# Kernel tuning notes

Measured on AMD Instinct MI355X. Metric: run time of the kernel, lower is better.

## Reference

```python
import jax, jax.numpy as jnp
from jax import lax
import numpy as np

HEAD_SIZE = 64
D_MIX = 32
D_DECAY = 64
D_GATE = 64


def setup_inputs() -> dict:
    key = jax.random.key(0)
    B, T, C = 4, 2048, 1024
    H = C // HEAD_SIZE
    ks = jax.random.split(key, 24)
    n = lambda i, shape, s=1.0: (jax.random.normal(ks[i], shape, dtype=jnp.float32) * s)
    return {
        "x": n(0, (B, T, C)),
        "maa_x": n(1, (C,), 0.1), "maa_w": n(2, (C,), 0.1), "maa_k": n(3, (C,), 0.1),
        "maa_v": n(4, (C,), 0.1), "maa_r": n(5, (C,), 0.1), "maa_g": n(6, (C,), 0.1),
        "maa_w1": n(7, (C, 5 * D_MIX), 0.01), "maa_w2": n(8, (5, D_MIX, C), 0.01),
        "Wr": n(9, (C, C), C ** -0.5), "Wk": n(10, (C, C), C ** -0.5),
        "Wv": n(11, (C, C), C ** -0.5), "Wo": n(12, (C, C), C ** -0.5),
        "gate_w1": n(13, (C, D_GATE), 0.01), "gate_w2": n(14, (D_GATE, C), 0.01),
        "time_decay": n(15, (C,), 1.0) - 4.0,
        "decay_w1": n(16, (C, D_DECAY), 0.01), "decay_w2": n(17, (D_DECAY, C), 0.01),
        "u": n(18, (H, HEAD_SIZE), 0.1),
        "ln_g": jnp.ones((C,), jnp.float32), "ln_b": jnp.zeros((C,), jnp.float32),
    }


def _wkv6(r, k, v, w, u):
    # r,k,v: [B,T,C]; w: decay (already exp(-exp(.))) [B,T,C]; u: [H,N]
    B, T, C = r.shape
    N = HEAD_SIZE
    H = C // N
    to_h = lambda a: a.reshape(B, T, H, N).transpose(1, 0, 2, 3)  # [T,B,H,N]
    rT, kT, vT, wT = map(to_h, (r, k, v, w))

    def step(S, inp):  # S: [B,H,N,N] (key_dim i x value_dim j)
        rt, kt, vt, wt = inp
        kv = kt[..., :, None] * vt[..., None, :]            # [B,H,N,N]
        y = jnp.einsum('bhi,bhij->bhj', rt, S + u[None, :, :, None] * kv)
        S = wt[..., None] * S + kv
        return S, y

    S0 = jnp.zeros((B, H, N, N), r.dtype)
    _, y = lax.scan(step, S0, (rT, kT, vT, wT))
    return y.transpose(1, 0, 2, 3).reshape(B, T, C)


def reference(x, maa_x, maa_w, maa_k, maa_v, maa_r, maa_g, maa_w1, maa_w2,
              Wr, Wk, Wv, Wo, gate_w1, gate_w2, time_decay, decay_w1, decay_w2,
              u, ln_g, ln_b):
    B, T, C = x.shape
    H, N = C // HEAD_SIZE, HEAD_SIZE
    # time shift: prepend zero row, drop last (ZeroPad2d((0,0,1,-1)))
    xx = jnp.concatenate([jnp.zeros_like(x[:, :1]), x[:, :-1]], axis=1) - x
    xxx = x + xx * maa_x
    lora = jnp.tanh(xxx @ maa_w1).reshape(B, T, 5, D_MIX)
    m = jnp.einsum('btfd,fdc->fbtc', lora, maa_w2)  # [5,B,T,C]
    mw, mk, mv, mr, mg = m[0], m[1], m[2], m[3], m[4]
    xw = x + xx * (maa_w + mw)
    xk = x + xx * (maa_k + mk)
    xv = x + xx * (maa_v + mv)
    xr = x + xx * (maa_r + mr)
    xg = x + xx * (maa_g + mg)
    r = xr @ Wr
    k = xk @ Wk
    v = xv @ Wv
    g = jnp.tanh(xg @ gate_w1) @ gate_w2
    w = time_decay + jnp.tanh(xw @ decay_w1) @ decay_w2
    wdec = jnp.exp(-jnp.exp(w))  # decay applied inside the CUDA kernel
    y = _wkv6(r, k, v, wdec, u)
    # GroupNorm over heads, eps = 1e-5 * HEAD_SIZE_DIVISOR**2 = 6.4e-4
    yh = y.reshape(B, T, H, N)
    mu = yh.mean(-1, keepdims=True)
    var = yh.var(-1, keepdims=True)
    yn = ((yh - mu) / jnp.sqrt(var + 6.4e-4)).reshape(B, T, C) * ln_g + ln_b
    return (yn * g) @ Wo
```

## Files before the change

### kernel.cpp

```cpp
#include <hip/hip_runtime.h>
#include <hip/hip_bf16.h>
#include <stdint.h>

typedef __hip_bfloat16 bf16;
typedef __attribute__((ext_vector_type(8))) short bf16x8;
typedef __attribute__((ext_vector_type(4))) float f32x4;

#define CC 1024
#define TT 2048
#define BB 4
#define BT 8192
#define HH 16
#define NN 64

#define MFMA(a, b, c) __builtin_amdgcn_mfma_f32_16x16x32_bf16(a, b, c, 0, 0, 0)

#define GLD(g, l) __builtin_amdgcn_global_load_lds( \
    (const __attribute__((address_space(1))) void*)(g), \
    (__attribute__((address_space(3))) void*)(l), 16, 0, 0)

__device__ __forceinline__ short f2bs(float f) {
    bf16 h = __float2bfloat16(f);
    return *reinterpret_cast<short*>(&h);
}
__device__ __forceinline__ float bs2f(short s) {
    bf16 h = *reinterpret_cast<bf16*>(&s);
    return __bfloat162float(h);
}

template <typename EPI>
__device__ __forceinline__ void gemm128(short* As, short* Bs,
                                        const bf16* __restrict__ A, int lda,
                                        const bf16* __restrict__ Bt, int ldb,
                                        int kiters, int m0, int n0, EPI epi)
{
    const int tid = threadIdx.x;
    const int l   = tid & 63, wv = tid >> 6;
    const int wm  = wv >> 1, wn = wv & 1;
    const int q   = l >> 4, lr = l & 15;
    const int row = tid & 127, kg1 = tid >> 7;

    f32x4 acc[4][4] = {};

    const bf16* ga = A  + (size_t)(m0 + row) * lda + kg1 * 8;
    const bf16* gb = Bt + (size_t)(n0 + row) * ldb + kg1 * 8;
    short* la1 = As + tid * 8;
    short* la2 = As + (tid + 256) * 8;
    short* lb1 = Bs + tid * 8;
    short* lb2 = Bs + (tid + 256) * 8;

    for (int kb = 0; kb < kiters; ++kb) {
        __syncthreads();
        const bf16* gak = ga + kb * 32;
        const bf16* gbk = gb + kb * 32;
        GLD(gak,      la1);
        GLD(gak + 16, la2);
        GLD(gbk,      lb1);
        GLD(gbk + 16, lb2);
        __syncthreads();
        bf16x8 af[4], bfb[4];
#pragma unroll
        for (int mt = 0; mt < 4; ++mt)
            af[mt] = *(const bf16x8*)(As + (q * 128 + wm * 64 + mt * 16 + lr) * 8);
#pragma unroll
        for (int nt = 0; nt < 4; ++nt)
            bfb[nt] = *(const bf16x8*)(Bs + (q * 128 + wn * 64 + nt * 16 + lr) * 8);
#pragma unroll
        for (int mt = 0; mt < 4; ++mt)
#pragma unroll
            for (int nt = 0; nt < 4; ++nt)
                acc[mt][nt] = MFMA(af[mt], bfb[nt], acc[mt][nt]);
    }
#pragma unroll
    for (int mt = 0; mt < 4; ++mt)
#pragma unroll
        for (int nt = 0; nt < 4; ++nt)
#pragma unroll
            for (int rr = 0; rr < 4; ++rr)
                epi(m0 + wm * 64 + mt * 16 + q * 4 + rr,
                    n0 + wn * 64 + nt * 16 + lr, acc[mt][nt][rr]);
}

template <typename EPI>
__device__ __forceinline__ void gemm128k64(short* As, short* Bs,
                                           const bf16* __restrict__ A, int lda,
                                           const bf16* __restrict__ Bt, int ldb,
                                           int kiters, int m0, int n0, EPI epi)
{
    const int tid = threadIdx.x;
    const int l   = tid & 63, wv = tid >> 6;
    const int wm  = wv >> 1, wn = wv & 1;
    const int q   = l >> 4, lr = l & 15;
    const int row = tid & 127, kg1 = tid >> 7;

    f32x4 acc[4][4] = {};

    const bf16* ga = A  + (size_t)(m0 + row) * lda + kg1 * 8;
    const bf16* gb = Bt + (size_t)(n0 + row) * ldb + kg1 * 8;

    for (int kb = 0; kb < kiters; ++kb) {
        __syncthreads();
        const bf16* gak = ga + kb * 64;
        const bf16* gbk = gb + kb * 64;
        GLD(gak,      As + tid * 8);
        GLD(gak + 16, As + (tid + 256) * 8);
        GLD(gak + 32, As + (tid + 512) * 8);
        GLD(gak + 48, As + (tid + 768) * 8);
        GLD(gbk,      Bs + tid * 8);
        GLD(gbk + 16, Bs + (tid + 256) * 8);
        GLD(gbk + 32, Bs + (tid + 512) * 8);
        GLD(gbk + 48, Bs + (tid + 768) * 8);
        __syncthreads();
        bf16x8 af[2][4], bfb[2][4];
#pragma unroll
        for (int hh = 0; hh < 2; ++hh) {
#pragma unroll
            for (int mt = 0; mt < 4; ++mt)
                af[hh][mt] = *(const bf16x8*)(As +
                    ((q + hh * 4) * 128 + wm * 64 + mt * 16 + lr) * 8);
#pragma unroll
            for (int nt = 0; nt < 4; ++nt)
                bfb[hh][nt] = *(const bf16x8*)(Bs +
                    ((q + hh * 4) * 128 + wn * 64 + nt * 16 + lr) * 8);
        }
#pragma unroll
        for (int mt = 0; mt < 4; ++mt)
#pragma unroll
            for (int nt = 0; nt < 4; ++nt) {
                acc[mt][nt] = MFMA(af[0][mt], bfb[0][nt], acc[mt][nt]);
                acc[mt][nt] = MFMA(af[1][mt], bfb[1][nt], acc[mt][nt]);
            }
    }
#pragma unroll
    for (int mt = 0; mt < 4; ++mt)
#pragma unroll
        for (int nt = 0; nt < 4; ++nt)
#pragma unroll
            for (int rr = 0; rr < 4; ++rr)
                epi(m0 + wm * 64 + mt * 16 + q * 4 + rr,
                    n0 + wn * 64 + nt * 16 + lr, acc[mt][nt][rr]);
}

__global__ __launch_bounds__(256) void k_prep_all(
    const float* __restrict__ Wr, const float* __restrict__ Wk,
    const float* __restrict__ Wv, const float* __restrict__ Wo,
    const float* __restrict__ maa_w1, const float* __restrict__ gate_w1,
    const float* __restrict__ decay_w1, const float* __restrict__ gate_w2,
    const float* __restrict__ decay_w2, const float* __restrict__ maa_w2,
    const float* __restrict__ mw, const float* __restrict__ mk,
    const float* __restrict__ mv, const float* __restrict__ mr,
    const float* __restrict__ mg, const float* __restrict__ x,
    const float* __restrict__ maa_x,
    bf16* __restrict__ WT3, bf16* __restrict__ WoT, bf16* __restrict__ w1T,
    bf16* __restrict__ w1T2, bf16* __restrict__ w2T2, bf16* __restrict__ w2T5,
    float* __restrict__ maas, bf16* __restrict__ xxx,
    bf16* __restrict__ xb, bf16* __restrict__ xxb)
{
    __shared__ float tile[32][33];
    int idx = blockIdx.x;
    if (idx >= 4900) {
        size_t i = ((size_t)(idx - 4900) * 256 + threadIdx.x) * 4;
        int cc = i & (CC - 1);
        int t  = (i >> 10) & (TT - 1);
        float4 xm = *(const float4*)(x + i);
        float4 xp = t ? *(const float4*)(x + i - CC)
                      : make_float4(0.f, 0.f, 0.f, 0.f);
        float4 ax = *(const float4*)(maa_x + cc);
        float xxv[4] = {xp.x - xm.x, xp.y - xm.y, xp.z - xm.z, xp.w - xm.w};
        float xmv[4] = {xm.x, xm.y, xm.z, xm.w};
        float axv[4] = {ax.x, ax.y, ax.z, ax.w};
#pragma unroll
        for (int e = 0; e < 4; ++e) {
            xb[i + e]  = __float2bfloat16(xmv[e]);
            xxb[i + e] = __float2bfloat16(xxv[e]);
            xxx[i + e] = __float2bfloat16(xmv[e] + xxv[e] * axv[e]);
        }
        return;
    }
    const float* src; bf16* dst; int rows, cols_in, tx_;
    if (idx < 4096) {
        int s = idx >> 10; idx &= 1023;
        src = (s == 0) ? Wr : (s == 1) ? Wk : (s == 2) ? Wv : Wo;
        dst = (s == 3) ? WoT : WT3 + (size_t)s * CC * CC;
        rows = CC; cols_in = CC; tx_ = 32;
    } else if (idx < 4352) { idx -= 4096; src = maa_w1;  dst = w1T;  rows = CC; cols_in = 160; tx_ = 8; }
    else if (idx < 4480)   { idx -= 4352; src = gate_w1; dst = w1T2; rows = CC; cols_in = 64;  tx_ = 4; }
    else if (idx < 4608)   { idx -= 4480; src = decay_w1; dst = w1T2 + 128 * CC; rows = CC; cols_in = 64; tx_ = 4; }
    else if (idx < 4672)   { idx -= 4608; src = gate_w2;  dst = w2T2;           rows = 64; cols_in = CC; tx_ = 32; }
    else if (idx < 4736)   { idx -= 4672; src = decay_w2; dst = w2T2 + CC * 64; rows = 64; cols_in = CC; tx_ = 32; }
    else if (idx < 4896)   { idx -= 4736; int f = idx >> 5; idx &= 31;
                             src = maa_w2 + (size_t)f * 32 * CC;
                             dst = w2T5 + (size_t)f * CC * 32; rows = 32; cols_in = CC; tx_ = 32; }
    else {
        int i = (idx - 4896) * 256 + threadIdx.x;
        if (i < CC) {
            maas[i]          = mw[i];
            maas[CC + i]     = mk[i];
            maas[2 * CC + i] = mv[i];
            maas[3 * CC + i] = mr[i];
            maas[4 * CC + i] = mg[i];
        }
        return;
    }
    int bx = idx % tx_, by = idx / tx_;
    int c0 = bx * 32, r0 = by * 32;
    int tx = threadIdx.x & 31, ty = threadIdx.x >> 5;
    for (int i = ty; i < 32; i += 8) {
        int cc2 = c0 + tx;
        tile[i][tx] = (cc2 < cols_in) ? src[(size_t)(r0 + i) * cols_in + cc2] : 0.f;
    }
    __syncthreads();
    for (int i = ty; i < 32; i += 8)
        dst[(size_t)(c0 + i) * rows + r0 + tx] = __float2bfloat16(tile[tx][i]);
}

__global__ __launch_bounds__(256) void g_lora(const bf16* __restrict__ xxx,
                                              const bf16* __restrict__ w1T,
                                              bf16* __restrict__ L)
{
    __shared__ __align__(16) short lds[8192];
    int m0 = blockIdx.x * 128, n0 = blockIdx.y * 128;
    gemm128(lds, lds + 4096, xxx, CC, w1T, CC, CC / 32, m0, n0,
            [&](int m, int n, float v) {
                if (n < 160) L[(size_t)m * 160 + n] = __float2bfloat16(tanhf(v));
            });
}

__global__ __launch_bounds__(256) void g_xvar(const bf16* __restrict__ L,
                                              const bf16* __restrict__ w2T,
                                              const float* __restrict__ maas,
                                              const bf16* __restrict__ xb,
                                              const bf16* __restrict__ xxb,
                                              bf16* __restrict__ xvars)
{
    __shared__ __align__(16) short lds[8192];
    int m0 = blockIdx.x * 128, n0 = blockIdx.y * 128;
    for (int f = 0; f < 5; ++f) {
        const bf16* A  = L + f * 32;
        const bf16* Bt = w2T + (size_t)f * CC * 32;
        const float* maa = maas + f * CC;
        bf16* out = xvars + (size_t)f * BT * CC;
        gemm128(lds, lds + 4096, A, 160, Bt, 32, 1, m0, n0,
                [&](int m, int n, float v) {
                    float xm = __bfloat162float(xb[(size_t)m * CC + n]);
                    float xx = __bfloat162float(xxb[(size_t)m * CC + n]);
                    out[(size_t)m * CC + n] =
                        __float2bfloat16(xm + xx * (maa[n] + v));
                });
    }
}

__global__ __launch_bounds__(256) void g_rkv5(const bf16* __restrict__ xvars,
                                              const bf16* __restrict__ WT,
                                              const bf16* __restrict__ w1T2,
                                              bf16* __restrict__ rkv,
                                              bf16* __restrict__ hid)
{
    __shared__ __align__(16) short lds[16384];
    int z = blockIdx.z;
    int m0 = blockIdx.x * 128;
    if (blockIdx.y < 8) {
        int n0 = blockIdx.y * 128;
        int f = (z == 0) ? 3 : z;
        const bf16* A  = xvars + (size_t)f * BT * CC;
        const bf16* Bt = WT + (size_t)z * CC * CC;
        bf16* out = rkv + (size_t)z * BT * CC;
        gemm128k64(lds, lds + 8192, A, CC, Bt, CC, CC / 64, m0, n0,
                   [&](int m, int n, float v) {
                       out[(size_t)m * CC + n] = __float2bfloat16(v);
                   });
    } else {
        if (z == 2) return;
        int zz = z;
        const bf16* A  = xvars + (size_t)(zz == 0 ? 4 : 0) * BT * CC;
        const bf16* Bt = w1T2 + (size_t)zz * 128 * CC;
        bf16* out = hid + (size_t)zz * BT * 64;
        gemm128k64(lds, lds + 8192, A, CC, Bt, CC, CC / 64, m0, 0,
                   [&](int m, int n, float v) {
                       if (n < 64) out[(size_t)m * 64 + n] = __float2bfloat16(tanhf(v));
                   });
    }
}

__global__ __launch_bounds__(256) void k_wkv_p1(const bf16* __restrict__ r,
                                                const bf16* __restrict__ kk,
                                                const bf16* __restrict__ vv,
                                                const bf16* __restrict__ hidW,
                                                const bf16* __restrict__ w2d,
                                                const float* __restrict__ td,
                                                const float* __restrict__ u,
                                                bf16* __restrict__ y,
                                                bf16* __restrict__ RTg,
                                                short* __restrict__ Mg,
                                                float* __restrict__ plg)
{
    constexpr int PW = 65, PB = 72;
    __shared__ __align__(16) char smem[16640 + 3 * 9216 + 768];
    float* LW = (float*)smem;
    short* VT = (short*)smem;
    short* RT = (short*)(smem + 16640);
    short* KT = (short*)(smem + 16640 + 9216);
    short* AT = KT;
    short* KH = (short*)(smem + 16640 + 2 * 9216);
    short* HT = KT;
    short* WD = KH;
    float* SU = (float*)(smem + 16640 + 3 * 9216);
    float* SD = SU + 64;

    const int tid = threadIdx.x;
    const int lane = tid & 63, wq = tid >> 6;
    const int row = tid >> 2, g = tid & 3, j0 = g * 16;
    const int l15 = lane & 15, q = lane >> 4;
    const int bh = blockIdx.x >> 5, c = blockIdx.x & 31;
    const int b = bh >> 4, h = bh & 15;
    const size_t base = (size_t)b * TT * CC + (size_t)h * NN;
    const int t0 = c * 64;
    const int bt0 = b * TT + t0;
    const size_t cb = (size_t)blockIdx.x * 4096;

    if (tid < 64) SU[tid] = u[h * NN + tid];

#pragma unroll
    for (int rnd = 0; rnd < 2; ++rnd) {
        int ee = rnd * 256 + tid;
        int rw = ee >> 3, c8 = (ee & 7) * 8;
        *(bf16x8*)(HT + rw * PB + c8) =
            *(const bf16x8*)(hidW + (size_t)(bt0 + rw) * 64 + c8);
        *(bf16x8*)(WD + rw * PB + c8) =
            *(const bf16x8*)(w2d + (size_t)(h * 64 + rw) * 64 + c8);
    }
    const size_t gb = base + (size_t)(t0 + row) * CC + j0;
    bf16x8 r0 = *(const bf16x8*)(r + gb),  r1 = *(const bf16x8*)(r + gb + 8);
    bf16x8 k0 = *(const bf16x8*)(kk + gb), k1 = *(const bf16x8*)(kk + gb + 8);
    bf16x8 v0 = *(const bf16x8*)(vv + gb), v1 = *(const bf16x8*)(vv + gb + 8);
    float tdv[4];
#pragma unroll
    for (int ct = 0; ct < 4; ++ct) tdv[ct] = td[h * 64 + ct * 16 + l15];
    __syncthreads();
    {
        bf16x8 aH0 = *(const bf16x8*)(HT + (wq * 16 + l15) * PB + q * 8);
        bf16x8 aH1 = *(const bf16x8*)(HT + (wq * 16 + l15) * PB + q * 8 + 32);
        f32x4 lwa[4] = {};
#pragma unroll
        for (int ct = 0; ct < 4; ++ct) {
            bf16x8 bW0 = *(const bf16x8*)(WD + (ct * 16 + l15) * PB + q * 8);
            bf16x8 bW1 = *(const bf16x8*)(WD + (ct * 16 + l15) * PB + q * 8 + 32);
            lwa[ct] = MFMA(aH0, bW0, lwa[ct]);
            lwa[ct] = MFMA(aH1, bW1, lwa[ct]);
        }
#pragma unroll
        for (int ct = 0; ct < 4; ++ct)
#pragma unroll
            for (int rr = 0; rr < 4; ++rr) {
                int t = wq * 16 + q * 4 + rr, j = ct * 16 + l15;
                LW[t * PW + j] = -expf(tdv[ct] + lwa[ct][rr]);
            }
    }
    __syncthreads();
    for (int jj = 0; jj < 16; ++jj) {
        int j = wq * 16 + jj;
        float xv = LW[lane * PW + j];
#pragma unroll
        for (int d = 1; d < 64; d <<= 1) {
            float t2 = __shfl_up(xv, d);
            if (lane >= d) xv += t2;
        }
        LW[lane * PW + j] = xv;
    }
    __syncthreads();
    float rF[16], kF[16];
#pragma unroll
    for (int c2 = 0; c2 < 8; ++c2) {
        rF[c2] = bs2f(r0[c2]); rF[8 + c2] = bs2f(r1[c2]);
        kF[c2] = bs2f(k0[c2]); kF[8 + c2] = bs2f(k1[c2]);
    }
    float cwp[16], cwm[16], cwL[16];
#pragma unroll
    for (int c2 = 0; c2 < 16; ++c2) {
        cwp[c2] = LW[row * PW + j0 + c2];
        cwm[c2] = row ? LW[(row - 1) * PW + j0 + c2] : 0.f;
        cwL[c2] = LW[63 * PW + j0 + c2];
    }
    bf16x8 w0, w1;
#pragma unroll
    for (int c2 = 0; c2 < 8; ++c2) {
        w0[c2] = f2bs(rF[c2] * expf(cwm[c2]));
        w1[c2] = f2bs(rF[8 + c2] * expf(cwm[8 + c2]));
    }
    *(bf16x8*)(RT + row * PB + j0)     = w0;
    *(bf16x8*)(RT + row * PB + j0 + 8) = w1;
    *(bf16x8*)((short*)RTg + cb + row * 64 + j0)     = w0;
    *(bf16x8*)((short*)RTg + cb + row * 64 + j0 + 8) = w1;
#pragma unroll
    for (int c2 = 0; c2 < 8; ++c2) {
        w0[c2] = f2bs(kF[c2] * expf(-cwp[c2]));
        w1[c2] = f2bs(kF[8 + c2] * expf(-cwp[8 + c2]));
    }
    *(bf16x8*)(KT + row * PB + j0)     = w0;
    *(bf16x8*)(KT + row * PB + j0 + 8) = w1;
#pragma unroll
    for (int c2 = 0; c2 < 16; ++c2)
        KH[(j0 + c2) * PB + row] = f2bs(kF[c2] * expf(cwL[c2] - cwp[c2]));
    if (tid < 64) plg[(size_t)blockIdx.x * 64 + tid] = expf(LW[63 * PW + tid]);
    float dpart = 0.f;
#pragma unroll
    for (int c2 = 0; c2 < 16; ++c2)
        dpart = fmaf(rF[c2] * kF[c2], SU[j0 + c2], dpart);
    dpart += __shfl_xor(dpart, 1);
    dpart += __shfl_xor(dpart, 2);
    if (g == 0) SD[row] = dpart;
    __syncthreads();
#pragma unroll
    for (int c2 = 0; c2 < 8; ++c2) {
        VT[(j0 + c2) * PB + row]     = v0[c2];
        VT[(j0 + 8 + c2) * PB + row] = v1[c2];
    }
    bf16x8 aF0 = *(const bf16x8*)(RT + (wq * 16 + l15) * PB + q * 8);
    bf16x8 aF1 = *(const bf16x8*)(RT + (wq * 16 + l15) * PB + q * 8 + 32);
    f32x4 Am[4] = {};
#pragma unroll
    for (int ct = 0; ct < 4; ++ct) {
        bf16x8 bF0 = *(const bf16x8*)(KT + (ct * 16 + l15) * PB + q * 8);
        bf16x8 bF1 = *(const bf16x8*)(KT + (ct * 16 + l15) * PB + q * 8 + 32);
        Am[ct] = MFMA(aF0, bF0, Am[ct]);
        Am[ct] = MFMA(aF1, bF1, Am[ct]);
    }
    __syncthreads();
#pragma unroll
    for (int ct = 0; ct < 4; ++ct)
#pragma unroll
        for (int rr = 0; rr < 4; ++rr) {
            int s = wq * 16 + q * 4 + rr, p = ct * 16 + l15;
            float vA = Am[ct][rr];
            vA = (p > s) ? 0.f : (p == s ? SD[s] : vA);
            AT[s * PB + p] = f2bs(vA);
        }
    __syncthreads();
    f32x4 Y[4] = {}, M[4] = {};
    bf16x8 aA0 = *(const bf16x8*)(AT + (wq * 16 + l15) * PB + q * 8);
    bf16x8 aA1 = *(const bf16x8*)(AT + (wq * 16 + l15) * PB + q * 8 + 32);
    bf16x8 aV0 = *(const bf16x8*)(VT + (wq * 16 + l15) * PB + q * 8);
    bf16x8 aV1 = *(const bf16x8*)(VT + (wq * 16 + l15) * PB + q * 8 + 32);
#pragma unroll
    for (int ct = 0; ct < 4; ++ct) {
        bf16x8 bV0 = *(const bf16x8*)(VT + (ct * 16 + l15) * PB + q * 8);
        bf16x8 bV1 = *(const bf16x8*)(VT + (ct * 16 + l15) * PB + q * 8 + 32);
        Y[ct] = MFMA(aA0, bV0, Y[ct]);
        Y[ct] = MFMA(aA1, bV1, Y[ct]);
        bf16x8 bK0 = *(const bf16x8*)(KH + (ct * 16 + l15) * PB + q * 8);
        bf16x8 bK1 = *(const bf16x8*)(KH + (ct * 16 + l15) * PB + q * 8 + 32);
        M[ct] = MFMA(aV0, bK0, M[ct]);
        M[ct] = MFMA(aV1, bK1, M[ct]);
    }
#pragma unroll
    for (int ct = 0; ct < 4; ++ct)
#pragma unroll
        for (int rr = 0; rr < 4; ++rr) {
            int s = wq * 16 + q * 4 + rr;
            y[base + (size_t)(t0 + s) * CC + ct * 16 + l15] =
                __float2bfloat16(Y[ct][rr]);
            Mg[cb + (size_t)s * 64 + ct * 16 + l15] = f2bs(M[ct][rr]);
        }
}

__global__ __launch_bounds__(256) void k_wkv_p2(const short* __restrict__ Mg,
                                                const float* __restrict__ plg,
                                                bf16* __restrict__ Sg)
{
    int bh = blockIdx.x >> 4, part = blockIdx.x & 15;
    int i = part * 4 + (threadIdx.x >> 6), j = threadIdx.x & 63;
    float S = 0.f;
    size_t eb = (size_t)bh * 32 * 4096 + (size_t)i * 64 + j;
    size_t pb = (size_t)bh * 32 * 64 + j;
    for (int c = 0; c < 32; ++c) {
        Sg[eb + (size_t)c * 4096] = __float2bfloat16(S);
        S = plg[pb + (size_t)c * 64] * S + bs2f(Mg[eb + (size_t)c * 4096]);
    }
}

__global__ __launch_bounds__(256) void k_wkv_p3(const bf16* __restrict__ RTg,
                                                const bf16* __restrict__ Sg,
                                                const bf16* __restrict__ y,
                                                const bf16* __restrict__ hidG,
                                                const bf16* __restrict__ w2g,
                                                const float* __restrict__ ln_g,
                                                const float* __restrict__ ln_b,
                                                bf16* __restrict__ A2)
{
    constexpr int PB = 72;
    __shared__ __align__(16) short BufA[64 * PB], BufB[64 * PB];
    const int tid = threadIdx.x;
    const int lane = tid & 63, wq = tid >> 6;
    const int l15 = lane & 15, q = lane >> 4;
    const int bh = blockIdx.x >> 5, c = blockIdx.x & 31;
    const int b = bh >> 4, h = bh & 15;
    const int t0 = c * 64;
    const int bt0 = b * TT + t0;
    const size_t cb = (size_t)blockIdx.x * 4096;

#pragma unroll
    for (int rnd = 0; rnd < 2; ++rnd) {
        int ee = rnd * 256 + tid;
        int rw = ee >> 3, c8 = (ee & 7) * 8;
        *(bf16x8*)(BufA + rw * PB + c8) =
            *(const bf16x8*)(hidG + (size_t)(bt0 + rw) * 64 + c8);
        *(bf16x8*)(BufB + rw * PB + c8) =
            *(const bf16x8*)(w2g + (size_t)(h * 64 + rw) * 64 + c8);
    }
    __syncthreads();
    f32x4 G[4] = {};
    {
        bf16x8 aH0 = *(const bf16x8*)(BufA + (wq * 16 + l15) * PB + q * 8);
        bf16x8 aH1 = *(const bf16x8*)(BufA + (wq * 16 + l15) * PB + q * 8 + 32);
#pragma unroll
        for (int ct = 0; ct < 4; ++ct) {
            bf16x8 bW0 = *(const bf16x8*)(BufB + (ct * 16 + l15) * PB + q * 8);
            bf16x8 bW1 = *(const bf16x8*)(BufB + (ct * 16 + l15) * PB + q * 8 + 32);
            G[ct] = MFMA(aH0, bW0, G[ct]);
            G[ct] = MFMA(aH1, bW1, G[ct]);
        }
    }
    __syncthreads();
#pragma unroll
    for (int rnd = 0; rnd < 2; ++rnd) {
        int ee = rnd * 256 + tid;
        int rw = ee >> 3, c8 = (ee & 7) * 8;
        *(bf16x8*)(BufA + rw * PB + c8) =
            *(const bf16x8*)((const short*)RTg + cb + rw * 64 + c8);
        *(bf16x8*)(BufB + rw * PB + c8) =
            *(const bf16x8*)((const short*)Sg + cb + rw * 64 + c8);
    }
    __syncthreads();

    f32x4 Yc[4];
#pragma unroll
    for (int ct = 0; ct < 4; ++ct)
#pragma unroll
        for (int rr = 0; rr < 4; ++rr) {
            int s = wq * 16 + q * 4 + rr;
            Yc[ct][rr] = __bfloat162float(
                y[((size_t)bt0 + s) * CC + h * NN + ct * 16 + l15]);
        }
    bf16x8 aF0 = *(const bf16x8*)(BufA + (wq * 16 + l15) * PB + q * 8);
    bf16x8 aF1 = *(const bf16x8*)(BufA + (wq * 16 + l15) * PB + q * 8 + 32);
#pragma unroll
    for (int ct = 0; ct < 4; ++ct) {
        bf16x8 bS0 = *(const bf16x8*)(BufB + (ct * 16 + l15) * PB + q * 8);
        bf16x8 bS1 = *(const bf16x8*)(BufB + (ct * 16 + l15) * PB + q * 8 + 32);
        Yc[ct] = MFMA(aF0, bS0, Yc[ct]);
        Yc[ct] = MFMA(aF1, bS1, Yc[ct]);
    }
#pragma unroll
    for (int rr = 0; rr < 4; ++rr) {
        float s1 = 0.f, s2 = 0.f;
#pragma unroll
        for (int ct = 0; ct < 4; ++ct) {
            float vA = Yc[ct][rr];
            s1 += vA; s2 += vA * vA;
        }
#pragma unroll
        for (int o = 1; o < 16; o <<= 1) {
            s1 += __shfl_xor(s1, o);
            s2 += __shfl_xor(s2, o);
        }
        float mu  = s1 * (1.f / 64.f);
        float var = s2 * (1.f / 64.f) - mu * mu;
        float rstd = rsqrtf(var + 6.4e-4f);
        int s = wq * 16 + q * 4 + rr;
        size_t mrow = ((size_t)bt0 + s) * CC;
#pragma unroll
        for (int ct = 0; ct < 4; ++ct) {
            int ch = h * NN + ct * 16 + l15;
            float yn = (Yc[ct][rr] - mu) * rstd;
            float out = (yn * ln_g[ch] + ln_b[ch]) * G[ct][rr];
            A2[mrow + ch] = __float2bfloat16(out);
        }
    }
}

__global__ __launch_bounds__(256) void g_out(const bf16* __restrict__ A2,
                                             const bf16* __restrict__ WoT,
                                             float* __restrict__ out)
{
    __shared__ __align__(16) short lds[16384];
    int m0 = blockIdx.x * 128, n0 = blockIdx.y * 128;
    gemm128k64(lds, lds + 8192, A2, CC, WoT, CC, CC / 64, m0, n0,
               [&](int m, int n, float v) { out[(size_t)m * CC + n] = v; });
}

extern "C" void kernel_launch(void* const* d_in, const int* in_sizes, int n_in,
                              void* d_out, int out_size, void* d_ws, size_t ws_size,
                              hipStream_t stream)
{
    const float* x        = (const float*)d_in[0];
    const float* maa_x    = (const float*)d_in[1];
    const float* maa_w    = (const float*)d_in[2];
    const float* maa_k    = (const float*)d_in[3];
    const float* maa_v    = (const float*)d_in[4];
    const float* maa_r    = (const float*)d_in[5];
    const float* maa_g    = (const float*)d_in[6];
    const float* maa_w1   = (const float*)d_in[7];
    const float* maa_w2   = (const float*)d_in[8];
    const float* Wr       = (const float*)d_in[9];
    const float* Wk       = (const float*)d_in[10];
    const float* Wv       = (const float*)d_in[11];
    const float* Wo       = (const float*)d_in[12];
    const float* gate_w1  = (const float*)d_in[13];
    const float* gate_w2  = (const float*)d_in[14];
    const float* time_dec = (const float*)d_in[15];
    const float* decay_w1 = (const float*)d_in[16];
    const float* decay_w2 = (const float*)d_in[17];
    const float* u        = (const float*)d_in[18];
    const float* ln_g     = (const float*)d_in[19];
    const float* ln_b     = (const float*)d_in[20];

    size_t off = 0;
    auto alloc = [&](size_t bytes) {
        off = (off + 255) & ~(size_t)255;
        void* p = (char*)d_ws + off;
        off += bytes;
        return p;
    };
    bf16*  WT3   = (bf16*) alloc(3ull * CC * CC * 2);
    bf16*  WoT   = (bf16*) alloc((size_t)CC * CC * 2);
    bf16*  w1T   = (bf16*) alloc(256ull * CC * 2);
    bf16*  w1T2  = (bf16*) alloc(2ull * 128 * CC * 2);
    bf16*  w2T2  = (bf16*) alloc(2ull * CC * 64 * 2);
    bf16*  w2T5  = (bf16*) alloc(5ull * CC * 32 * 2);
    float* maas  = (float*)alloc(5ull * CC * 4);
    char* bufA = (char*)alloc((size_t)BT * CC * 2);
    bf16* xxxbf = (bf16*)bufA;
    bf16* A2    = (bf16*)bufA;
    char* bufB = (char*)alloc((size_t)BT * 160 * 2);
    bf16* Lbf  = (bf16*)bufB;
    bf16* hid  = (bf16*)bufB;
    char* bufC = (char*)alloc(5ull * BT * CC * 2);
    bf16*  xvars = (bf16*)bufC;
    bf16*  ybuf  = (bf16*)bufC;
    bf16*  RTg   = (bf16*)(bufC + (size_t)BT * CC * 2);
    bf16*  rkv  = (bf16*)alloc(3ull * BT * CC * 2);
    bf16*  Sg   = rkv;
    bf16*  xb   = (bf16*) alloc((size_t)BT * CC * 2);
    bf16*  xxb  = (bf16*) alloc((size_t)BT * CC * 2);
    short* Mg   = (short*)alloc(64ull * 32 * 4096 * 2);
    float* plg  = (float*)alloc(64ull * 32 * 64 * 4);

    k_prep_all<<<dim3(13092), 256, 0, stream>>>(
        Wr, Wk, Wv, Wo, maa_w1, gate_w1, decay_w1, gate_w2, decay_w2, maa_w2,
        maa_w, maa_k, maa_v, maa_r, maa_g, x, maa_x,
        WT3, WoT, w1T, w1T2, w2T2, w2T5, maas, xxxbf, xb, xxb);

    g_lora<<<dim3(64, 2), 256, 0, stream>>>(xxxbf, w1T, Lbf);
    g_xvar<<<dim3(64, 8), 256, 0, stream>>>(Lbf, w2T5, maas, xb, xxb, xvars);
    g_rkv5<<<dim3(64, 9, 3), 256, 0, stream>>>(xvars, WT3, w1T2, rkv, hid);
    k_wkv_p1<<<dim3(2048), 256, 0, stream>>>(rkv, rkv + (size_t)BT * CC,
                                             rkv + 2ull * BT * CC,
                                             hid + (size_t)BT * 64,
                                             w2T2 + CC * 64,
                                             time_dec, u, ybuf, RTg, Mg, plg);
    k_wkv_p2<<<dim3(1024), 256, 0, stream>>>(Mg, plg, Sg);
    k_wkv_p3<<<dim3(2048), 256, 0, stream>>>(RTg, Sg, ybuf,
                                             hid,
                                             w2T2,
                                             ln_g, ln_b, A2);
    g_out<<<dim3(64, 8), 256, 0, stream>>>(A2, WoT, (float*)d_out);
}
```

Baseline: 419.3 us.

## Double-buffer LDS tiles in k64 GEMM to overlap loads with MFMA

Turns the 128x128x64 GEMM main loop into a two-stage software pipeline. The next k-tile is issued via global_load_lds into an alternate LDS buffer while MFMAs run on the current one, and the MFMA block runs at raised wave priority via s_setprio. This is meant to hide global-load latency and cut one barrier per iteration. In exchange LDS per block doubles to 64KB, which may reduce occupancy for the rkv and output GEMMs.

```diff
diff --git a/kernel.cpp b/kernel.cpp
--- a/kernel.cpp
+++ b/kernel.cpp
@@ -98,31 +98,42 @@
     const bf16* ga = A  + (size_t)(m0 + row) * lda + kg1 * 8;
     const bf16* gb = Bt + (size_t)(n0 + row) * ldb + kg1 * 8;
 
-    for (int kb = 0; kb < kiters; ++kb) {
-        __syncthreads();
+    auto stage = [&](int kb, int u) {
         const bf16* gak = ga + kb * 64;
         const bf16* gbk = gb + kb * 64;
-        GLD(gak,      As + tid * 8);
-        GLD(gak + 16, As + (tid + 256) * 8);
-        GLD(gak + 32, As + (tid + 512) * 8);
-        GLD(gak + 48, As + (tid + 768) * 8);
-        GLD(gbk,      Bs + tid * 8);
-        GLD(gbk + 16, Bs + (tid + 256) * 8);
-        GLD(gbk + 32, Bs + (tid + 512) * 8);
-        GLD(gbk + 48, Bs + (tid + 768) * 8);
-        __syncthreads();
+        short* la = As + u * 8192 + tid * 8;
+        short* lb = Bs + u * 8192 + tid * 8;
+        GLD(gak,      la);
+        GLD(gak + 16, la + 2048);
+        GLD(gak + 32, la + 4096);
+        GLD(gak + 48, la + 6144);
+        GLD(gbk,      lb);
+        GLD(gbk + 16, lb + 2048);
+        GLD(gbk + 32, lb + 4096);
+        GLD(gbk + 48, lb + 6144);
+    };
+
+    __syncthreads();
+    stage(0, 0);
+    __syncthreads();
+    for (int kb = 0; kb < kiters; ++kb) {
+        const int cur = kb & 1;
+        if (kb + 1 < kiters) stage(kb + 1, cur ^ 1);
+        const short* Ac = As + cur * 8192;
+        const short* Bc = Bs + cur * 8192;
         bf16x8 af[2][4], bfb[2][4];
 #pragma unroll
         for (int hh = 0; hh < 2; ++hh) {
 #pragma unroll
             for (int mt = 0; mt < 4; ++mt)
-                af[hh][mt] = *(const bf16x8*)(As +
+                af[hh][mt] = *(const bf16x8*)(Ac +
                     ((q + hh * 4) * 128 + wm * 64 + mt * 16 + lr) * 8);
 #pragma unroll
             for (int nt = 0; nt < 4; ++nt)
-                bfb[hh][nt] = *(const bf16x8*)(Bs +
+                bfb[hh][nt] = *(const bf16x8*)(Bc +
                     ((q + hh * 4) * 128 + wn * 64 + nt * 16 + lr) * 8);
         }
+        __builtin_amdgcn_s_setprio(1);
 #pragma unroll
         for (int mt = 0; mt < 4; ++mt)
 #pragma unroll
@@ -130,6 +141,8 @@
                 acc[mt][nt] = MFMA(af[0][mt], bfb[0][nt], acc[mt][nt]);
                 acc[mt][nt] = MFMA(af[1][mt], bfb[1][nt], acc[mt][nt]);
             }
+        __builtin_amdgcn_s_setprio(0);
+        __syncthreads();
     }
 #pragma unroll
     for (int mt = 0; mt < 4; ++mt)
@@ -256,7 +269,7 @@
                                               bf16* __restrict__ rkv,
                                               bf16* __restrict__ hid)
 {
-    __shared__ __align__(16) short lds[16384];
+    __shared__ __align__(16) short lds[32768];
     int z = blockIdx.z;
     int m0 = blockIdx.x * 128;
     if (blockIdx.y < 8) {
@@ -265,7 +278,7 @@
         const bf16* A  = xvars + (size_t)f * BT * CC;
         const bf16* Bt = WT + (size_t)z * CC * CC;
         bf16* out = rkv + (size_t)z * BT * CC;
-        gemm128k64(lds, lds + 8192, A, CC, Bt, CC, CC / 64, m0, n0,
+        gemm128k64(lds, lds + 16384, A, CC, Bt, CC, CC / 64, m0, n0,
                    [&](int m, int n, float v) {
                        out[(size_t)m * CC + n] = __float2bfloat16(v);
                    });
@@ -275,7 +288,7 @@
         const bf16* A  = xvars + (size_t)(zz == 0 ? 4 : 0) * BT * CC;
         const bf16* Bt = w1T2 + (size_t)zz * 128 * CC;
         bf16* out = hid + (size_t)zz * BT * 64;
-        gemm128k64(lds, lds + 8192, A, CC, Bt, CC, CC / 64, m0, 0,
+        gemm128k64(lds, lds + 16384, A, CC, Bt, CC, CC / 64, m0, 0,
                    [&](int m, int n, float v) {
                        if (n < 64) out[(size_t)m * 64 + n] = __float2bfloat16(tanhf(v));
                    });
@@ -582,9 +595,9 @@
                                              const bf16* __restrict__ WoT,
                                              float* __restrict__ out)
 {
-    __shared__ __align__(16) short lds[16384];
+    __shared__ __align__(16) short lds[32768];
     int m0 = blockIdx.x * 128, n0 = blockIdx.y * 128;
-    gemm128k64(lds, lds + 8192, A2, CC, WoT, CC, CC / 64, m0, n0,
+    gemm128k64(lds, lds + 16384, A2, CC, WoT, CC, CC / 64, m0, n0,
                [&](int m, int n, float v) { out[(size_t)m * CC + n] = v; });
 }
 
```

Result: no change. 417.8 us (-0.3%).
